# Optimization experiments

Measured on AMD Instinct MI355X. Metric: run time of the kernel, lower is better.

Reference implementation:

```python
import jax, jax.numpy as jnp
import numpy as np

H = 1024
V = 50257
B = 64
T = 512


def setup_inputs() -> dict:
    key = jax.random.key(0)
    ks = jax.random.split(key, 16)
    s = 0.02
    return {
        "input_seq": jax.random.randint(ks[0], (B,), 0, V, dtype=jnp.int32),
        "last_hidden": jax.random.normal(ks[1], (1, B, H), dtype=jnp.float32),
        "encoder_outputs": jax.random.normal(ks[2], (B, T, H), dtype=jnp.float32),
        "emb": jax.random.normal(ks[3], (V, H), dtype=jnp.float32) * s,
        "W_ih": jax.random.normal(ks[4], (3 * H, H), dtype=jnp.float32) * s,
        "W_hh": jax.random.normal(ks[5], (3 * H, H), dtype=jnp.float32) * s,
        "b_ih": jnp.zeros((3 * H,), jnp.float32),
        "b_hh": jnp.zeros((3 * H,), jnp.float32),
        "W_a": jax.random.normal(ks[6], (H, H), dtype=jnp.float32) * s,
        "b_a": jnp.zeros((H,), jnp.float32),
        "W_c": jax.random.normal(ks[7], (H, 2 * H), dtype=jnp.float32) * s,
        "b_c": jnp.zeros((H,), jnp.float32),
        "W_o": jax.random.normal(ks[8], (V, H), dtype=jnp.float32) * s,
        "b_o": jnp.zeros((V,), jnp.float32),
    }


def reference(input_seq, last_hidden, encoder_outputs, emb, W_ih, W_hh, b_ih, b_hh,
              W_a, b_a, W_c, b_c, W_o, b_o):
    # Embedding lookup (dropout is identity in eval)
    x = emb[input_seq]                      # [B, H]
    h0 = last_hidden[0]                     # [B, H] (num_layers == 1)

    # Single GRU step, torch gate order (r, z, n)
    gi = x @ W_ih.T + b_ih                  # [B, 3H]
    gh = h0 @ W_hh.T + b_hh                 # [B, 3H]
    r = jax.nn.sigmoid(gi[:, :H] + gh[:, :H])
    z = jax.nn.sigmoid(gi[:, H:2 * H] + gh[:, H:2 * H])
    n = jnp.tanh(gi[:, 2 * H:] + r * gh[:, 2 * H:])
    h = (1.0 - z) * n + z * h0              # [B, H]

    # Attention, method='general': batched (replaces per-batch torch.mm loop)
    energy = jnp.einsum('bth,oh->bto', encoder_outputs, W_a) + b_a  # [B, T, H]
    scores = jnp.einsum('bh,bth->bt', h, energy)                    # [B, T]
    attn_w = jax.nn.softmax(scores, axis=1)                         # [B, T]
    context = jnp.einsum('bt,bth->bh', attn_w, encoder_outputs)     # [B, H]

    concat_input = jnp.concatenate([h, context], axis=1)            # [B, 2H]
    concat_output = jnp.tanh(concat_input @ W_c.T + b_c)            # [B, H]
    output = concat_output @ W_o.T + b_o                            # [B, V]
    hidden = h[None]                                                # [1, B, H]
    return (output, hidden)
```

## Files before the change

### kernel.cpp

```cpp
#include <hip/hip_runtime.h>
#include <hip/hip_bf16.h>
#include <cstdint>
#include <cstddef>

#define H 1024
#define V 50257
#define B 64
#define T 512

typedef __attribute__((ext_vector_type(8))) short bf16x8;
typedef __attribute__((ext_vector_type(4))) float f32x4;

__device__ __forceinline__ float sigmoidf_(float x) { return 1.0f / (1.0f + expf(-x)); }

__device__ __forceinline__ unsigned short f2bf_rn(float x) {
    __hip_bfloat16 h = __float2bfloat16(x);
    return __builtin_bit_cast(unsigned short, h);
}

__device__ __forceinline__ void gl_lds16(const float* g, float* l) {
    __builtin_amdgcn_global_load_lds(
        (const __attribute__((address_space(1))) unsigned*)g,
        (__attribute__((address_space(3))) unsigned*)l, 16, 0, 0);
}

__device__ __forceinline__ void wait_vm8() {
    asm volatile("s_waitcnt vmcnt(8)" ::: "memory");
    __builtin_amdgcn_sched_barrier(0);
}
__device__ __forceinline__ void wait_vm0() {
    asm volatile("s_waitcnt vmcnt(0)" ::: "memory");
    __builtin_amdgcn_sched_barrier(0);
}
__device__ __forceinline__ void lds_war_guard() {
    asm volatile("s_waitcnt lgkmcnt(0)" ::: "memory");
    __builtin_amdgcn_sched_barrier(0);
}

__global__ __launch_bounds__(256) void k_gates(const int* __restrict__ seq,
                                               const float* __restrict__ emb,
                                               const float* __restrict__ h0,
                                               const float* __restrict__ Wih,
                                               const float* __restrict__ Whh,
                                               float* __restrict__ Pgi,
                                               float* __restrict__ Pgh) {
    __shared__ __align__(16) float Bs[2][128 * 64];
    const int z = blockIdx.z;
    const float* Bm = z ? Whh : Wih;
    float* C = (z ? Pgh : Pgi) + (size_t)blockIdx.y * 64 * (3 * H);
    const int t = threadIdx.x;
    const int w = t >> 6, lane = t & 63;
    const int li = lane & 15, qu = lane >> 4;
    const int n0 = blockIdx.x * 128;
    const int k0 = blockIdx.y * 256;
    const int N = 3 * H;

    const float* Arow[4];
#pragma unroll
    for (int ms = 0; ms < 4; ++ms) {
        int m = ms * 16 + li;
        Arow[ms] = z ? (h0 + (size_t)m * H) : (emb + (size_t)seq[m] * H);
    }

    f32x4 acc[4][2];
#pragma unroll
    for (int ms = 0; ms < 4; ++ms)
#pragma unroll
        for (int nt = 0; nt < 2; ++nt) acc[ms][nt] = (f32x4){0.f, 0.f, 0.f, 0.f};

#define STG(BUF, KK)                                                            \
    {                                                                           \
        _Pragma("unroll")                                                       \
        for (int j = 0; j < 8; ++j) {                                           \
            int cidx = (w * 8 + j) * 64 + lane;                                 \
            int row = cidx >> 4, cs = cidx & 15;                                \
            int cg = cs ^ (row & 15);                                           \
            const float* gp = Bm + (size_t)(n0 + row) * H + (KK) + cg * 4;      \
            gl_lds16(gp, &Bs[BUF][(w * 8 + j) * 256]);                          \
        }                                                                       \
    }

#define CONSUME(BUF, KK)                                                        \
    {                                                                           \
        _Pragma("unroll")                                                       \
        for (int ks = 0; ks < 2; ++ks) {                                        \
            bf16x8 af[4];                                                       \
            _Pragma("unroll")                                                   \
            for (int ms = 0; ms < 4; ++ms) {                                    \
                float4 a0 = *(const float4*)&Arow[ms][(KK) + ks * 32 + qu * 8]; \
                float4 a1 = *(const float4*)&Arow[ms][(KK) + ks * 32 + qu * 8 + 4]; \
                af[ms][0] = (short)f2bf_rn(a0.x); af[ms][1] = (short)f2bf_rn(a0.y); \
                af[ms][2] = (short)f2bf_rn(a0.z); af[ms][3] = (short)f2bf_rn(a0.w); \
                af[ms][4] = (short)f2bf_rn(a1.x); af[ms][5] = (short)f2bf_rn(a1.y); \
                af[ms][6] = (short)f2bf_rn(a1.z); af[ms][7] = (short)f2bf_rn(a1.w); \
            }                                                                   \
            _Pragma("unroll")                                                   \
            for (int nt = 0; nt < 2; ++nt) {                                    \
                int row = w * 32 + nt * 16 + li;                                \
                int cc0 = ks * 8 + qu * 2;                                      \
                float4 x0 = *(const float4*)&Bs[BUF][row * 64 + ((cc0)     ^ (row & 15)) * 4]; \
                float4 x1 = *(const float4*)&Bs[BUF][row * 64 + ((cc0 + 1) ^ (row & 15)) * 4]; \
                bf16x8 bfr;                                                     \
                bfr[0] = (short)f2bf_rn(x0.x); bfr[1] = (short)f2bf_rn(x0.y);   \
                bfr[2] = (short)f2bf_rn(x0.z); bfr[3] = (short)f2bf_rn(x0.w);   \
                bfr[4] = (short)f2bf_rn(x1.x); bfr[5] = (short)f2bf_rn(x1.y);   \
                bfr[6] = (short)f2bf_rn(x1.z); bfr[7] = (short)f2bf_rn(x1.w);   \
                _Pragma("unroll")                                               \
                for (int ms = 0; ms < 4; ++ms)                                  \
                    acc[ms][nt] = __builtin_amdgcn_mfma_f32_16x16x32_bf16(      \
                        af[ms], bfr, acc[ms][nt], 0, 0, 0);                     \
            }                                                                   \
        }                                                                       \
    }

    STG(0, k0)
    STG(1, k0 + 64)
    for (int kt = 0; kt < 3; ++kt) {
        const int buf = kt & 1;
        wait_vm8();
        CONSUME(buf, k0 + kt * 64)
        if (kt + 2 < 4) { lds_war_guard(); STG(buf, k0 + (kt + 2) * 64) }
    }
    wait_vm0();
    CONSUME(1, k0 + 3 * 64)
#undef STG
#undef CONSUME

#pragma unroll
    for (int nt = 0; nt < 2; ++nt) {
        int col = n0 + w * 32 + nt * 16 + li;
#pragma unroll
        for (int ms = 0; ms < 4; ++ms)
#pragma unroll
            for (int j = 0; j < 4; ++j)
                C[(size_t)(ms * 16 + qu * 4 + j) * N + col] = acc[ms][nt][j];
    }
}

__global__ __launch_bounds__(256) void k_mfma_bt(const unsigned short* __restrict__ A,
                                                 int lda,
                                                 const float* __restrict__ Bm, int ldb,
                                                 float* __restrict__ Cp, int N, int KC) {
    __shared__ __align__(16) float Bs[2][128 * 64];
    float* C = Cp + (size_t)blockIdx.y * 64 * N;
    const int t = threadIdx.x;
    const int w = t >> 6, lane = t & 63;
    const int li = lane & 15, qu = lane >> 4;
    const int n0 = blockIdx.x * 128;
    const int k0 = blockIdx.y * KC;
    const int nsteps = KC >> 6;

    f32x4 acc[4][2];
#pragma unroll
    for (int ms = 0; ms < 4; ++ms)
#pragma unroll
        for (int nt = 0; nt < 2; ++nt) acc[ms][nt] = (f32x4){0.f, 0.f, 0.f, 0.f};

#define STG(BUF, KK)                                                            \
    {                                                                           \
        _Pragma("unroll")                                                       \
        for (int j = 0; j < 8; ++j) {                                           \
            int cidx = (w * 8 + j) * 64 + lane;                                 \
            int row = cidx >> 4, cs = cidx & 15;                                \
            int cg = cs ^ (row & 15);                                           \
            const float* gp = Bm + (size_t)(n0 + row) * ldb + (KK) + cg * 4;    \
            gl_lds16(gp, &Bs[BUF][(w * 8 + j) * 256]);                          \
        }                                                                       \
    }

#define CONSUME(BUF, KK)                                                        \
    {                                                                           \
        _Pragma("unroll")                                                       \
        for (int ks = 0; ks < 2; ++ks) {                                        \
            bf16x8 af[4];                                                       \
            _Pragma("unroll")                                                   \
            for (int ms = 0; ms < 4; ++ms)                                      \
                af[ms] = *(const bf16x8*)&A[(size_t)(ms * 16 + li) * lda + (KK) + ks * 32 + qu * 8]; \
            _Pragma("unroll")                                                   \
            for (int nt = 0; nt < 2; ++nt) {                                    \
                int row = w * 32 + nt * 16 + li;                                \
                int cc0 = ks * 8 + qu * 2;                                      \
                float4 x0 = *(const float4*)&Bs[BUF][row * 64 + ((cc0)     ^ (row & 15)) * 4]; \
                float4 x1 = *(const float4*)&Bs[BUF][row * 64 + ((cc0 + 1) ^ (row & 15)) * 4]; \
                bf16x8 bfr;                                                     \
                bfr[0] = (short)f2bf_rn(x0.x); bfr[1] = (short)f2bf_rn(x0.y);   \
                bfr[2] = (short)f2bf_rn(x0.z); bfr[3] = (short)f2bf_rn(x0.w);   \
                bfr[4] = (short)f2bf_rn(x1.x); bfr[5] = (short)f2bf_rn(x1.y);   \
                bfr[6] = (short)f2bf_rn(x1.z); bfr[7] = (short)f2bf_rn(x1.w);   \
                _Pragma("unroll")                                               \
                for (int ms = 0; ms < 4; ++ms)                                  \
                    acc[ms][nt] = __builtin_amdgcn_mfma_f32_16x16x32_bf16(      \
                        af[ms], bfr, acc[ms][nt], 0, 0, 0);                     \
            }                                                                   \
        }                                                                       \
    }

    STG(0, k0)
    STG(1, k0 + 64)
    for (int kt = 0; kt < nsteps - 1; ++kt) {
        const int buf = kt & 1;
        wait_vm8();
        CONSUME(buf, k0 + kt * 64)
        if (kt + 2 < nsteps) { lds_war_guard(); STG(buf, k0 + (kt + 2) * 64) }
    }
    wait_vm0();
    CONSUME((nsteps - 1) & 1, k0 + (nsteps - 1) * 64)
#undef STG
#undef CONSUME

#pragma unroll
    for (int nt = 0; nt < 2; ++nt) {
        int col = n0 + w * 32 + nt * 16 + li;
#pragma unroll
        for (int ms = 0; ms < 4; ++ms)
#pragma unroll
            for (int j = 0; j < 4; ++j)
                C[(size_t)(ms * 16 + qu * 4 + j) * N + col] = acc[ms][nt][j];
    }
}

__global__ __launch_bounds__(256) void k_mfma_wa(const unsigned short* __restrict__ cat_bf,
                                                 const float* __restrict__ Wa,
                                                 float* __restrict__ Pu) {
    const int t = threadIdx.x;
    const int w = t >> 6, lane = t & 63;
    const int li = lane & 15, qu = lane >> 4;
    const int n0 = blockIdx.x * 64;
    const int k0 = blockIdx.y * 128;

    f32x4 acc[4];
#pragma unroll
    for (int ms = 0; ms < 4; ++ms) acc[ms] = (f32x4){0.f, 0.f, 0.f, 0.f};

    const int col = n0 + w * 16 + li;

    for (int kt = 0; kt < 2; ++kt) {
        const int kk = k0 + kt * 64;
#pragma unroll
        for (int ks = 0; ks < 2; ++ks) {
            bf16x8 af[4];
#pragma unroll
            for (int ms = 0; ms < 4; ++ms)
                af[ms] = *(const bf16x8*)&cat_bf[(size_t)(ms * 16 + li) * 2048 + kk + ks * 32 + qu * 8];
            const int kb = kk + ks * 32 + qu * 8;
            bf16x8 bfr;
#pragma unroll
            for (int e = 0; e < 8; ++e)
                bfr[e] = (short)f2bf_rn(Wa[(size_t)(kb + e) * H + col]);
#pragma unroll
            for (int ms = 0; ms < 4; ++ms)
                acc[ms] = __builtin_amdgcn_mfma_f32_16x16x32_bf16(
                    af[ms], bfr, acc[ms], 0, 0, 0);
        }
    }
    float* C = Pu + (size_t)blockIdx.y * 64 * H;
#pragma unroll
    for (int ms = 0; ms < 4; ++ms)
#pragma unroll
        for (int j = 0; j < 4; ++j)
            C[(size_t)(ms * 16 + qu * 4 + j) * H + col] = acc[ms][j];
}

__global__ void k_gru(const float* __restrict__ Pgi, const float* __restrict__ Pgh,
                      const float* __restrict__ bih, const float* __restrict__ bhh,
                      const float* __restrict__ h0, unsigned short* __restrict__ cat_bf,
                      float* __restrict__ hid) {
    int i = blockIdx.x * 256 + threadIdx.x;
    int b = i >> 10, h = i & 1023;
    float gr = bih[h], gz = bih[H + h], gn = bih[2 * H + h];
    float hr = bhh[h], hz = bhh[H + h], hn = bhh[2 * H + h];
#pragma unroll
    for (int kt = 0; kt < 4; ++kt) {
        const float* pi = Pgi + (size_t)kt * B * 3 * H + (size_t)b * 3 * H;
        const float* ph = Pgh + (size_t)kt * B * 3 * H + (size_t)b * 3 * H;
        gr += pi[h]; gz += pi[H + h]; gn += pi[2 * H + h];
        hr += ph[h]; hz += ph[H + h]; hn += ph[2 * H + h];
    }
    float r = sigmoidf_(gr + hr);
    float z = sigmoidf_(gz + hz);
    float n = tanhf(gn + r * hn);
    float hv = (1.0f - z) * n + z * h0[i];
    cat_bf[(size_t)b * 2048 + h] = f2bf_rn(hv);
    hid[i] = hv;
}

__global__ __launch_bounds__(256) void k_flash(const float* __restrict__ Pu,
                                               const float* __restrict__ enc,
                                               float* __restrict__ Pm,
                                               float* __restrict__ Pl,
                                               float* __restrict__ Pc) {
    const int b = blockIdx.x >> 4, ch = blockIdx.x & 15;
    const int w = threadIdx.x >> 6, lane = threadIdx.x & 63;

    float4 uu[4];
#pragma unroll
    for (int it = 0; it < 4; ++it) {
        int col = (it * 64 + lane) * 4;
        float4 s = *(const float4*)&Pu[(size_t)b * H + col];
#pragma unroll
        for (int kt = 1; kt < 8; ++kt) {
            float4 p = *(const float4*)&Pu[(size_t)kt * B * H + (size_t)b * H + col];
            s.x += p.x; s.y += p.y; s.z += p.z; s.w += p.w;
        }
        uu[it] = s;
    }

    float m = -3.4e38f, l = 0.f;
    float4 c[4] = {{0,0,0,0},{0,0,0,0},{0,0,0,0},{0,0,0,0}};
    const float* ebase = enc + ((size_t)b * T + ch * 32 + w * 8) * H;

#pragma unroll 2
    for (int tt = 0; tt < 8; ++tt) {
        float4 e[4];
#pragma unroll
        for (int it = 0; it < 4; ++it)
            e[it] = *(const float4*)&ebase[(size_t)tt * H + (it * 64 + lane) * 4];
        float s = 0.f;
#pragma unroll
        for (int it = 0; it < 4; ++it)
            s += uu[it].x * e[it].x + uu[it].y * e[it].y +
                 uu[it].z * e[it].z + uu[it].w * e[it].w;
#pragma unroll
        for (int o = 32; o; o >>= 1) s += __shfl_xor(s, o, 64);
        float mn = fmaxf(m, s);
        float scale = __expf(m - mn);
        float p = __expf(s - mn);
        l = l * scale + p;
#pragma unroll
        for (int it = 0; it < 4; ++it) {
            c[it].x = fmaf(p, e[it].x, c[it].x * scale);
            c[it].y = fmaf(p, e[it].y, c[it].y * scale);
            c[it].z = fmaf(p, e[it].z, c[it].z * scale);
            c[it].w = fmaf(p, e[it].w, c[it].w * scale);
        }
        m = mn;
    }

    __shared__ float Lm[4], Ll[4];
    __shared__ __align__(16) float Lc[4][H];
#pragma unroll
    for (int it = 0; it < 4; ++it)
        *(float4*)&Lc[w][(it * 64 + lane) * 4] = c[it];
    if (lane == 0) { Lm[w] = m; Ll[w] = l; }
    __syncthreads();

    float M = fmaxf(fmaxf(Lm[0], Lm[1]), fmaxf(Lm[2], Lm[3]));
    float e0 = __expf(Lm[0] - M), e1 = __expf(Lm[1] - M),
          e2 = __expf(Lm[2] - M), e3 = __expf(Lm[3] - M);
    float L = Ll[0] * e0 + Ll[1] * e1 + Ll[2] * e2 + Ll[3] * e3;
    int col = threadIdx.x * 4;
    float4 c0 = *(const float4*)&Lc[0][col];
    float4 c1 = *(const float4*)&Lc[1][col];
    float4 c2 = *(const float4*)&Lc[2][col];
    float4 c3 = *(const float4*)&Lc[3][col];
    float4 cc;
    cc.x = c0.x * e0 + c1.x * e1 + c2.x * e2 + c3.x * e3;
    cc.y = c0.y * e0 + c1.y * e1 + c2.y * e2 + c3.y * e3;
    cc.z = c0.z * e0 + c1.z * e1 + c2.z * e2 + c3.z * e3;
    cc.w = c0.w * e0 + c1.w * e1 + c2.w * e2 + c3.w * e3;
    const int rec = blockIdx.x;
    if (threadIdx.x == 0) { Pm[rec] = M; Pl[rec] = L; }
    *(float4*)&Pc[(size_t)rec * H + col] = cc;
}

__global__ void k_fcomb(const float* __restrict__ Pm, const float* __restrict__ Pl,
                        const float* __restrict__ Pc, unsigned short* __restrict__ cat_bf) {
    const int b = blockIdx.x;
    const int col = threadIdx.x * 4;
    float M = -3.4e38f;
#pragma unroll
    for (int i = 0; i < 16; ++i) M = fmaxf(M, Pm[b * 16 + i]);
    float L = 0.f;
    float4 cc = {0, 0, 0, 0};
#pragma unroll 4
    for (int i = 0; i < 16; ++i) {
        float wgt = __expf(Pm[b * 16 + i] - M);
        L += Pl[b * 16 + i] * wgt;
        float4 p = *(const float4*)&Pc[(size_t)(b * 16 + i) * H + col];
        cc.x += wgt * p.x; cc.y += wgt * p.y;
        cc.z += wgt * p.z; cc.w += wgt * p.w;
    }
    float inv = 1.0f / L;
    ushort4 o;
    o.x = f2bf_rn(cc.x * inv); o.y = f2bf_rn(cc.y * inv);
    o.z = f2bf_rn(cc.z * inv); o.w = f2bf_rn(cc.w * inv);
    *(ushort4*)&cat_bf[(size_t)b * 2048 + 1024 + col] = o;
}

__global__ void k_co(const float* __restrict__ Pc, const float* __restrict__ bc,
                     unsigned short* __restrict__ co_bf) {
    int i = blockIdx.x * 256 + threadIdx.x;
    int h = i & 1023;
    float s = bc[h];
#pragma unroll
    for (int kt = 0; kt < 16; ++kt) s += Pc[kt * (B * H) + i];
    co_bf[i] = f2bf_rn(tanhf(s));
}

__global__ __launch_bounds__(256) void k_out_mfma(const unsigned short* __restrict__ co_bf,
                                                  const float* __restrict__ Wo,
                                                  const float* __restrict__ bo,
                                                  float* __restrict__ out) {
    __shared__ __align__(16) float Bs[2][128 * 64];
    const int t = threadIdx.x;
    const int w = t >> 6, lane = t & 63;
    const int li = lane & 15, qu = lane >> 4;
    const int v0 = blockIdx.x * 128;

    f32x4 acc[4][2];
#pragma unroll
    for (int ms = 0; ms < 4; ++ms)
#pragma unroll
        for (int nt = 0; nt < 2; ++nt) acc[ms][nt] = (f32x4){0.f, 0.f, 0.f, 0.f};

#define STAGE(BUF, KK)                                                          \
    {                                                                           \
        _Pragma("unroll")                                                       \
        for (int j = 0; j < 8; ++j) {                                           \
            int cidx = (w * 8 + j) * 64 + lane;                                 \
            int row = cidx >> 4, cs = cidx & 15;                                \
            int cg = cs ^ (row & 15);                                           \
            int vr = v0 + row; if (vr >= V) vr = V - 1;                         \
            const float* gp = Wo + (size_t)vr * H + (KK) + cg * 4;              \
            gl_lds16(gp, &Bs[BUF][(w * 8 + j) * 256]);                          \
        }                                                                       \
    }

#define CONSUME(BUF, KK)                                                        \
    {                                                                           \
        _Pragma("unroll")                                                       \
        for (int ks = 0; ks < 2; ++ks) {                                        \
            bf16x8 af[4];                                                       \
            _Pragma("unroll")                                                   \
            for (int ms = 0; ms < 4; ++ms)                                      \
                af[ms] = *(const bf16x8*)&co_bf[(size_t)(ms * 16 + li) * H + (KK) + ks * 32 + qu * 8]; \
            _Pragma("unroll")                                                   \
            for (int nt = 0; nt < 2; ++nt) {                                    \
                int row = w * 32 + nt * 16 + li;                                \
                int cc0 = ks * 8 + qu * 2;                                      \
                float4 x0 = *(const float4*)&Bs[BUF][row * 64 + ((cc0)     ^ (row & 15)) * 4]; \
                float4 x1 = *(const float4*)&Bs[BUF][row * 64 + ((cc0 + 1) ^ (row & 15)) * 4]; \
                bf16x8 bfr;                                                     \
                bfr[0] = (short)f2bf_rn(x0.x); bfr[1] = (short)f2bf_rn(x0.y);   \
                bfr[2] = (short)f2bf_rn(x0.z); bfr[3] = (short)f2bf_rn(x0.w);   \
                bfr[4] = (short)f2bf_rn(x1.x); bfr[5] = (short)f2bf_rn(x1.y);   \
                bfr[6] = (short)f2bf_rn(x1.z); bfr[7] = (short)f2bf_rn(x1.w);   \
                _Pragma("unroll")                                               \
                for (int ms = 0; ms < 4; ++ms)                                  \
                    acc[ms][nt] = __builtin_amdgcn_mfma_f32_16x16x32_bf16(      \
                        af[ms], bfr, acc[ms][nt], 0, 0, 0);                     \
            }                                                                   \
        }                                                                       \
    }

    STAGE(0, 0)
    STAGE(1, 64)
    for (int kt = 0; kt < 15; ++kt) {
        const int buf = kt & 1;
        wait_vm8();
        CONSUME(buf, kt * 64)
        if (kt + 2 < 16) { lds_war_guard(); STAGE(buf, (kt + 2) * 64) }
    }
    wait_vm0();
    CONSUME(1, 15 * 64)
#undef STAGE
#undef CONSUME

#pragma unroll
    for (int nt = 0; nt < 2; ++nt) {
        int v = v0 + w * 32 + nt * 16 + li;
        if (v < V) {
            float bov = bo[v];
#pragma unroll
            for (int ms = 0; ms < 4; ++ms)
#pragma unroll
                for (int j = 0; j < 4; ++j)
                    out[(size_t)(ms * 16 + qu * 4 + j) * V + v] = acc[ms][nt][j] + bov;
        }
    }
}

extern "C" void kernel_launch(void* const* d_in, const int* in_sizes, int n_in,
                              void* d_out, int out_size, void* d_ws, size_t ws_size,
                              hipStream_t stream) {
    (void)in_sizes; (void)n_in; (void)out_size; (void)ws_size;
    const int*   seq = (const int*)d_in[0];
    const float* h0  = (const float*)d_in[1];
    const float* enc = (const float*)d_in[2];
    const float* emb = (const float*)d_in[3];
    const float* Wih = (const float*)d_in[4];
    const float* Whh = (const float*)d_in[5];
    const float* bih = (const float*)d_in[6];
    const float* bhh = (const float*)d_in[7];
    const float* Wa  = (const float*)d_in[8];
    const float* Wc  = (const float*)d_in[10];
    const float* bc  = (const float*)d_in[11];
    const float* Wo  = (const float*)d_in[12];
    const float* bo  = (const float*)d_in[13];

    float* out = (float*)d_out;
    float* hid = out + (size_t)B * V;

    float* ws   = (float*)d_ws;
    float* Pgi  = ws;
    float* Pgh  = Pgi + 786432;
    float* Pu   = Pgh + 786432;
    float* Pm   = Pu + 524288;
    float* Pl   = Pm + 1024;
    float* Pc   = Pl + 1024;
    float* Pcg  = Pc + 1048576;
    unsigned short* cat_bf = (unsigned short*)(Pcg + 1048576);
    unsigned short* co_bf  = cat_bf + 131072;

    k_gates<<<dim3(24, 4, 2), 256, 0, stream>>>(seq, emb, h0, Wih, Whh, Pgi, Pgh);
    k_gru<<<256, 256, 0, stream>>>(Pgi, Pgh, bih, bhh, h0, cat_bf, hid);
    k_mfma_wa<<<dim3(16, 8), 256, 0, stream>>>(cat_bf, Wa, Pu);
    k_flash<<<1024, 256, 0, stream>>>(Pu, enc, Pm, Pl, Pc);
    k_fcomb<<<64, 256, 0, stream>>>(Pm, Pl, Pc, cat_bf);
    k_mfma_bt<<<dim3(8, 16), 256, 0, stream>>>(cat_bf, 2 * H, Wc, 2 * H, Pcg, H, 128);
    k_co<<<256, 256, 0, stream>>>(Pcg, bc, co_bf);
    k_out_mfma<<<(V + 127) / 128, 256, 0, stream>>>(co_bf, Wo, bo, out);
}
```

Before: 135.2 us.

## Fuse split-K reductions into producer kernels via last-block atomic counters

The flash-attention partial combine is merged into the flash kernel, and the Wc split-K reduction plus tanh into the Wc GEMM. In each case the last block to finish, detected with an atomic counter after a threadfence, does the combine. This removes two kernel launches and their launch gaps. The cost is a memset for the flags and a serialized tail in the last-arriving block.

```diff
diff --git a/kernel.cpp b/kernel.cpp
--- a/kernel.cpp
+++ b/kernel.cpp
@@ -137,18 +137,192 @@
     }
 }
 
-__global__ __launch_bounds__(256) void k_mfma_bt(const unsigned short* __restrict__ A,
-                                                 int lda,
-                                                 const float* __restrict__ Bm, int ldb,
-                                                 float* __restrict__ Cp, int N, int KC) {
+__global__ void k_gru(const float* __restrict__ Pgi, const float* __restrict__ Pgh,
+                      const float* __restrict__ bih, const float* __restrict__ bhh,
+                      const float* __restrict__ h0, unsigned short* __restrict__ cat_bf,
+                      float* __restrict__ hid) {
+    int i = blockIdx.x * 256 + threadIdx.x;
+    int b = i >> 10, h = i & 1023;
+    float gr = bih[h], gz = bih[H + h], gn = bih[2 * H + h];
+    float hr = bhh[h], hz = bhh[H + h], hn = bhh[2 * H + h];
+#pragma unroll
+    for (int kt = 0; kt < 4; ++kt) {
+        const float* pi = Pgi + (size_t)kt * B * 3 * H + (size_t)b * 3 * H;
+        const float* ph = Pgh + (size_t)kt * B * 3 * H + (size_t)b * 3 * H;
+        gr += pi[h]; gz += pi[H + h]; gn += pi[2 * H + h];
+        hr += ph[h]; hz += ph[H + h]; hn += ph[2 * H + h];
+    }
+    float r = sigmoidf_(gr + hr);
+    float z = sigmoidf_(gz + hz);
+    float n = tanhf(gn + r * hn);
+    float hv = (1.0f - z) * n + z * h0[i];
+    cat_bf[(size_t)b * 2048 + h] = f2bf_rn(hv);
+    hid[i] = hv;
+}
+
+__global__ __launch_bounds__(256) void k_mfma_wa(const unsigned short* __restrict__ cat_bf,
+                                                 const float* __restrict__ Wa,
+                                                 float* __restrict__ Pu) {
+    const int t = threadIdx.x;
+    const int w = t >> 6, lane = t & 63;
+    const int li = lane & 15, qu = lane >> 4;
+    const int n0 = blockIdx.x * 64;
+    const int k0 = blockIdx.y * 128;
+
+    f32x4 acc[4];
+#pragma unroll
+    for (int ms = 0; ms < 4; ++ms) acc[ms] = (f32x4){0.f, 0.f, 0.f, 0.f};
+
+    const int col = n0 + w * 16 + li;
+
+    for (int kt = 0; kt < 2; ++kt) {
+        const int kk = k0 + kt * 64;
+#pragma unroll
+        for (int ks = 0; ks < 2; ++ks) {
+            bf16x8 af[4];
+#pragma unroll
+            for (int ms = 0; ms < 4; ++ms)
+                af[ms] = *(const bf16x8*)&cat_bf[(size_t)(ms * 16 + li) * 2048 + kk + ks * 32 + qu * 8];
+            const int kb = kk + ks * 32 + qu * 8;
+            bf16x8 bfr;
+#pragma unroll
+            for (int e = 0; e < 8; ++e)
+                bfr[e] = (short)f2bf_rn(Wa[(size_t)(kb + e) * H + col]);
+#pragma unroll
+            for (int ms = 0; ms < 4; ++ms)
+                acc[ms] = __builtin_amdgcn_mfma_f32_16x16x32_bf16(
+                    af[ms], bfr, acc[ms], 0, 0, 0);
+        }
+    }
+    float* C = Pu + (size_t)blockIdx.y * 64 * H;
+#pragma unroll
+    for (int ms = 0; ms < 4; ++ms)
+#pragma unroll
+        for (int j = 0; j < 4; ++j)
+            C[(size_t)(ms * 16 + qu * 4 + j) * H + col] = acc[ms][j];
+}
+
+__global__ __launch_bounds__(256) void k_flash_fc(const float* __restrict__ Pu,
+                                                  const float* __restrict__ enc,
+                                                  float* __restrict__ Pm,
+                                                  float* __restrict__ Pl,
+                                                  float* __restrict__ Pc,
+                                                  unsigned short* __restrict__ cat_bf,
+                                                  int* __restrict__ flags) {
+    const int b = blockIdx.x >> 4, ch = blockIdx.x & 15;
+    const int w = threadIdx.x >> 6, lane = threadIdx.x & 63;
+
+    float4 uu[4];
+#pragma unroll
+    for (int it = 0; it < 4; ++it) {
+        int col = (it * 64 + lane) * 4;
+        float4 s = *(const float4*)&Pu[(size_t)b * H + col];
+#pragma unroll
+        for (int kt = 1; kt < 8; ++kt) {
+            float4 p = *(const float4*)&Pu[(size_t)kt * B * H + (size_t)b * H + col];
+            s.x += p.x; s.y += p.y; s.z += p.z; s.w += p.w;
+        }
+        uu[it] = s;
+    }
+
+    float m = -3.4e38f, l = 0.f;
+    float4 c[4] = {{0,0,0,0},{0,0,0,0},{0,0,0,0},{0,0,0,0}};
+    const float* ebase = enc + ((size_t)b * T + ch * 32 + w * 8) * H;
+
+#pragma unroll 2
+    for (int tt = 0; tt < 8; ++tt) {
+        float4 e[4];
+#pragma unroll
+        for (int it = 0; it < 4; ++it)
+            e[it] = *(const float4*)&ebase[(size_t)tt * H + (it * 64 + lane) * 4];
+        float s = 0.f;
+#pragma unroll
+        for (int it = 0; it < 4; ++it)
+            s += uu[it].x * e[it].x + uu[it].y * e[it].y +
+                 uu[it].z * e[it].z + uu[it].w * e[it].w;
+#pragma unroll
+        for (int o = 32; o; o >>= 1) s += __shfl_xor(s, o, 64);
+        float mn = fmaxf(m, s);
+        float scale = __expf(m - mn);
+        float p = __expf(s - mn);
+        l = l * scale + p;
+#pragma unroll
+        for (int it = 0; it < 4; ++it) {
+            c[it].x = fmaf(p, e[it].x, c[it].x * scale);
+            c[it].y = fmaf(p, e[it].y, c[it].y * scale);
+            c[it].z = fmaf(p, e[it].z, c[it].z * scale);
+            c[it].w = fmaf(p, e[it].w, c[it].w * scale);
+        }
+        m = mn;
+    }
+
+    __shared__ float Lm[4], Ll[4];
+    __shared__ __align__(16) float Lc[4][H];
+    __shared__ int isLast;
+#pragma unroll
+    for (int it = 0; it < 4; ++it)
+        *(float4*)&Lc[w][(it * 64 + lane) * 4] = c[it];
+    if (lane == 0) { Lm[w] = m; Ll[w] = l; }
+    __syncthreads();
+
+    float M = fmaxf(fmaxf(Lm[0], Lm[1]), fmaxf(Lm[2], Lm[3]));
+    float e0 = __expf(Lm[0] - M), e1 = __expf(Lm[1] - M),
+          e2 = __expf(Lm[2] - M), e3 = __expf(Lm[3] - M);
+    float L = Ll[0] * e0 + Ll[1] * e1 + Ll[2] * e2 + Ll[3] * e3;
+    int col = threadIdx.x * 4;
+    float4 c0 = *(const float4*)&Lc[0][col];
+    float4 c1 = *(const float4*)&Lc[1][col];
+    float4 c2 = *(const float4*)&Lc[2][col];
+    float4 c3 = *(const float4*)&Lc[3][col];
+    float4 cc;
+    cc.x = c0.x * e0 + c1.x * e1 + c2.x * e2 + c3.x * e3;
+    cc.y = c0.y * e0 + c1.y * e1 + c2.y * e2 + c3.y * e3;
+    cc.z = c0.z * e0 + c1.z * e1 + c2.z * e2 + c3.z * e3;
+    cc.w = c0.w * e0 + c1.w * e1 + c2.w * e2 + c3.w * e3;
+    const int rec = blockIdx.x;
+    if (threadIdx.x == 0) { Pm[rec] = M; Pl[rec] = L; }
+    *(float4*)&Pc[(size_t)rec * H + col] = cc;
+
+    __threadfence();
+    if (threadIdx.x == 0)
+        isLast = (atomicAdd(&flags[b], 1) == 15);
+    __syncthreads();
+    if (!isLast) return;
+    __threadfence();
+
+    float Mg = -3.4e38f;
+#pragma unroll
+    for (int i = 0; i < 16; ++i) Mg = fmaxf(Mg, Pm[b * 16 + i]);
+    float Lg = 0.f;
+    float4 ccg = {0, 0, 0, 0};
+#pragma unroll 4
+    for (int i = 0; i < 16; ++i) {
+        float wgt = __expf(Pm[b * 16 + i] - Mg);
+        Lg += Pl[b * 16 + i] * wgt;
+        float4 p = *(const float4*)&Pc[(size_t)(b * 16 + i) * H + col];
+        ccg.x += wgt * p.x; ccg.y += wgt * p.y;
+        ccg.z += wgt * p.z; ccg.w += wgt * p.w;
+    }
+    float inv = 1.0f / Lg;
+    ushort4 o;
+    o.x = f2bf_rn(ccg.x * inv); o.y = f2bf_rn(ccg.y * inv);
+    o.z = f2bf_rn(ccg.z * inv); o.w = f2bf_rn(ccg.w * inv);
+    *(ushort4*)&cat_bf[(size_t)b * 2048 + 1024 + col] = o;
+}
+
+__global__ __launch_bounds__(256) void k_wc_co(const unsigned short* __restrict__ A,
+                                               const float* __restrict__ Wc,
+                                               const float* __restrict__ bc,
+                                               float* __restrict__ Pcg,
+                                               unsigned short* __restrict__ co_bf,
+                                               int* __restrict__ flags) {
     __shared__ __align__(16) float Bs[2][128 * 64];
-    float* C = Cp + (size_t)blockIdx.y * 64 * N;
+    float* C = Pcg + (size_t)blockIdx.y * 64 * H;
     const int t = threadIdx.x;
     const int w = t >> 6, lane = t & 63;
     const int li = lane & 15, qu = lane >> 4;
     const int n0 = blockIdx.x * 128;
-    const int k0 = blockIdx.y * KC;
-    const int nsteps = KC >> 6;
+    const int k0 = blockIdx.y * 128;
 
     f32x4 acc[4][2];
 #pragma unroll
@@ -163,7 +337,7 @@
             int cidx = (w * 8 + j) * 64 + lane;                                 \
             int row = cidx >> 4, cs = cidx & 15;                                \
             int cg = cs ^ (row & 15);                                           \
-            const float* gp = Bm + (size_t)(n0 + row) * ldb + (KK) + cg * 4;    \
+            const float* gp = Wc + (size_t)(n0 + row) * (2 * H) + (KK) + cg * 4; \
             gl_lds16(gp, &Bs[BUF][(w * 8 + j) * 256]);                          \
         }                                                                       \
     }
@@ -175,7 +349,7 @@
             bf16x8 af[4];                                                       \
             _Pragma("unroll")                                                   \
             for (int ms = 0; ms < 4; ++ms)                                      \
-                af[ms] = *(const bf16x8*)&A[(size_t)(ms * 16 + li) * lda + (KK) + ks * 32 + qu * 8]; \
+                af[ms] = *(const bf16x8*)&A[(size_t)(ms * 16 + li) * 2048 + (KK) + ks * 32 + qu * 8]; \
             _Pragma("unroll")                                                   \
             for (int nt = 0; nt < 2; ++nt) {                                    \
                 int row = w * 32 + nt * 16 + li;                                \
@@ -197,14 +371,10 @@
 
     STG(0, k0)
     STG(1, k0 + 64)
-    for (int kt = 0; kt < nsteps - 1; ++kt) {
-        const int buf = kt & 1;
-        wait_vm8();
-        CONSUME(buf, k0 + kt * 64)
-        if (kt + 2 < nsteps) { lds_war_guard(); STG(buf, k0 + (kt + 2) * 64) }
-    }
+    wait_vm8();
+    CONSUME(0, k0)
     wait_vm0();
-    CONSUME((nsteps - 1) & 1, k0 + (nsteps - 1) * 64)
+    CONSUME(1, k0 + 64)
 #undef STG
 #undef CONSUME
 
@@ -215,186 +385,28 @@
         for (int ms = 0; ms < 4; ++ms)
 #pragma unroll
             for (int j = 0; j < 4; ++j)
-                C[(size_t)(ms * 16 + qu * 4 + j) * N + col] = acc[ms][nt][j];
-    }
-}
-
-__global__ __launch_bounds__(256) void k_mfma_wa(const unsigned short* __restrict__ cat_bf,
-                                                 const float* __restrict__ Wa,
-                                                 float* __restrict__ Pu) {
-    const int t = threadIdx.x;
-    const int w = t >> 6, lane = t & 63;
-    const int li = lane & 15, qu = lane >> 4;
-    const int n0 = blockIdx.x * 64;
-    const int k0 = blockIdx.y * 128;
-
-    f32x4 acc[4];
-#pragma unroll
-    for (int ms = 0; ms < 4; ++ms) acc[ms] = (f32x4){0.f, 0.f, 0.f, 0.f};
-
-    const int col = n0 + w * 16 + li;
-
-    for (int kt = 0; kt < 2; ++kt) {
-        const int kk = k0 + kt * 64;
-#pragma unroll
-        for (int ks = 0; ks < 2; ++ks) {
-            bf16x8 af[4];
-#pragma unroll
-            for (int ms = 0; ms < 4; ++ms)
-                af[ms] = *(const bf16x8*)&cat_bf[(size_t)(ms * 16 + li) * 2048 + kk + ks * 32 + qu * 8];
-            const int kb = kk + ks * 32 + qu * 8;
-            bf16x8 bfr;
-#pragma unroll
-            for (int e = 0; e < 8; ++e)
-                bfr[e] = (short)f2bf_rn(Wa[(size_t)(kb + e) * H + col]);
-#pragma unroll
-            for (int ms = 0; ms < 4; ++ms)
-                acc[ms] = __builtin_amdgcn_mfma_f32_16x16x32_bf16(
-                    af[ms], bfr, acc[ms], 0, 0, 0);
-        }
-    }
-    float* C = Pu + (size_t)blockIdx.y * 64 * H;
-#pragma unroll
-    for (int ms = 0; ms < 4; ++ms)
-#pragma unroll
-        for (int j = 0; j < 4; ++j)
-            C[(size_t)(ms * 16 + qu * 4 + j) * H + col] = acc[ms][j];
-}
-
-__global__ void k_gru(const float* __restrict__ Pgi, const float* __restrict__ Pgh,
-                      const float* __restrict__ bih, const float* __restrict__ bhh,
-                      const float* __restrict__ h0, unsigned short* __restrict__ cat_bf,
-                      float* __restrict__ hid) {
-    int i = blockIdx.x * 256 + threadIdx.x;
-    int b = i >> 10, h = i & 1023;
-    float gr = bih[h], gz = bih[H + h], gn = bih[2 * H + h];
-    float hr = bhh[h], hz = bhh[H + h], hn = bhh[2 * H + h];
-#pragma unroll
-    for (int kt = 0; kt < 4; ++kt) {
-        const float* pi = Pgi + (size_t)kt * B * 3 * H + (size_t)b * 3 * H;
-        const float* ph = Pgh + (size_t)kt * B * 3 * H + (size_t)b * 3 * H;
-        gr += pi[h]; gz += pi[H + h]; gn += pi[2 * H + h];
-        hr += ph[h]; hz += ph[H + h]; hn += ph[2 * H + h];
-    }
-    float r = sigmoidf_(gr + hr);
-    float z = sigmoidf_(gz + hz);
-    float n = tanhf(gn + r * hn);
-    float hv = (1.0f - z) * n + z * h0[i];
-    cat_bf[(size_t)b * 2048 + h] = f2bf_rn(hv);
-    hid[i] = hv;
-}
-
-__global__ __launch_bounds__(256) void k_flash(const float* __restrict__ Pu,
-                                               const float* __restrict__ enc,
-                                               float* __restrict__ Pm,
-                                               float* __restrict__ Pl,
-                                               float* __restrict__ Pc) {
-    const int b = blockIdx.x >> 4, ch = blockIdx.x & 15;
-    const int w = threadIdx.x >> 6, lane = threadIdx.x & 63;
-
-    float4 uu[4];
-#pragma unroll
-    for (int it = 0; it < 4; ++it) {
-        int col = (it * 64 + lane) * 4;
-        float4 s = *(const float4*)&Pu[(size_t)b * H + col];
-#pragma unroll
-        for (int kt = 1; kt < 8; ++kt) {
-            float4 p = *(const float4*)&Pu[(size_t)kt * B * H + (size_t)b * H + col];
-            s.x += p.x; s.y += p.y; s.z += p.z; s.w += p.w;
-        }
-        uu[it] = s;
-    }
-
-    float m = -3.4e38f, l = 0.f;
-    float4 c[4] = {{0,0,0,0},{0,0,0,0},{0,0,0,0},{0,0,0,0}};
-    const float* ebase = enc + ((size_t)b * T + ch * 32 + w * 8) * H;
-
-#pragma unroll 2
-    for (int tt = 0; tt < 8; ++tt) {
-        float4 e[4];
-#pragma unroll
-        for (int it = 0; it < 4; ++it)
-            e[it] = *(const float4*)&ebase[(size_t)tt * H + (it * 64 + lane) * 4];
-        float s = 0.f;
-#pragma unroll
-        for (int it = 0; it < 4; ++it)
-            s += uu[it].x * e[it].x + uu[it].y * e[it].y +
-                 uu[it].z * e[it].z + uu[it].w * e[it].w;
-#pragma unroll
-        for (int o = 32; o; o >>= 1) s += __shfl_xor(s, o, 64);
-        float mn = fmaxf(m, s);
-        float scale = __expf(m - mn);
-        float p = __expf(s - mn);
-        l = l * scale + p;
-#pragma unroll
-        for (int it = 0; it < 4; ++it) {
-            c[it].x = fmaf(p, e[it].x, c[it].x * scale);
-            c[it].y = fmaf(p, e[it].y, c[it].y * scale);
-            c[it].z = fmaf(p, e[it].z, c[it].z * scale);
-            c[it].w = fmaf(p, e[it].w, c[it].w * scale);
-        }
-        m = mn;
-    }
-
-    __shared__ float Lm[4], Ll[4];
-    __shared__ __align__(16) float Lc[4][H];
-#pragma unroll
-    for (int it = 0; it < 4; ++it)
-        *(float4*)&Lc[w][(it * 64 + lane) * 4] = c[it];
-    if (lane == 0) { Lm[w] = m; Ll[w] = l; }
+                C[(size_t)(ms * 16 + qu * 4 + j) * H + col] = acc[ms][nt][j];
+    }
+
+    __shared__ int isLast;
+    __threadfence();
+    if (t == 0)
+        isLast = (atomicAdd(&flags[blockIdx.x], 1) == 15);
     __syncthreads();
-
-    float M = fmaxf(fmaxf(Lm[0], Lm[1]), fmaxf(Lm[2], Lm[3]));
-    float e0 = __expf(Lm[0] - M), e1 = __expf(Lm[1] - M),
-          e2 = __expf(Lm[2] - M), e3 = __expf(Lm[3] - M);
-    float L = Ll[0] * e0 + Ll[1] * e1 + Ll[2] * e2 + Ll[3] * e3;
-    int col = threadIdx.x * 4;
-    float4 c0 = *(const float4*)&Lc[0][col];
-    float4 c1 = *(const float4*)&Lc[1][col];
-    float4 c2 = *(const float4*)&Lc[2][col];
-    float4 c3 = *(const float4*)&Lc[3][col];
-    float4 cc;
-    cc.x = c0.x * e0 + c1.x * e1 + c2.x * e2 + c3.x * e3;
-    cc.y = c0.y * e0 + c1.y * e1 + c2.y * e2 + c3.y * e3;
-    cc.z = c0.z * e0 + c1.z * e1 + c2.z * e2 + c3.z * e3;
-    cc.w = c0.w * e0 + c1.w * e1 + c2.w * e2 + c3.w * e3;
-    const int rec = blockIdx.x;
-    if (threadIdx.x == 0) { Pm[rec] = M; Pl[rec] = L; }
-    *(float4*)&Pc[(size_t)rec * H + col] = cc;
-}
-
-__global__ void k_fcomb(const float* __restrict__ Pm, const float* __restrict__ Pl,
-                        const float* __restrict__ Pc, unsigned short* __restrict__ cat_bf) {
-    const int b = blockIdx.x;
-    const int col = threadIdx.x * 4;
-    float M = -3.4e38f;
-#pragma unroll
-    for (int i = 0; i < 16; ++i) M = fmaxf(M, Pm[b * 16 + i]);
-    float L = 0.f;
-    float4 cc = {0, 0, 0, 0};
+    if (!isLast) return;
+    __threadfence();
+
+#pragma unroll
+    for (int e = 0; e < 32; ++e) {
+        int elem = e * 256 + t;
+        int m_ = elem >> 7, c_ = elem & 127;
+        int n = n0 + c_;
+        float s = bc[n];
 #pragma unroll 4
-    for (int i = 0; i < 16; ++i) {
-        float wgt = __expf(Pm[b * 16 + i] - M);
-        L += Pl[b * 16 + i] * wgt;
-        float4 p = *(const float4*)&Pc[(size_t)(b * 16 + i) * H + col];
-        cc.x += wgt * p.x; cc.y += wgt * p.y;
-        cc.z += wgt * p.z; cc.w += wgt * p.w;
-    }
-    float inv = 1.0f / L;
-    ushort4 o;
-    o.x = f2bf_rn(cc.x * inv); o.y = f2bf_rn(cc.y * inv);
-    o.z = f2bf_rn(cc.z * inv); o.w = f2bf_rn(cc.w * inv);
-    *(ushort4*)&cat_bf[(size_t)b * 2048 + 1024 + col] = o;
-}
-
-__global__ void k_co(const float* __restrict__ Pc, const float* __restrict__ bc,
-                     unsigned short* __restrict__ co_bf) {
-    int i = blockIdx.x * 256 + threadIdx.x;
-    int h = i & 1023;
-    float s = bc[h];
-#pragma unroll
-    for (int kt = 0; kt < 16; ++kt) s += Pc[kt * (B * H) + i];
-    co_bf[i] = f2bf_rn(tanhf(s));
+        for (int kt = 0; kt < 16; ++kt)
+            s += Pcg[(size_t)kt * B * H + (size_t)m_ * H + n];
+        co_bf[(size_t)m_ * H + n] = f2bf_rn(tanhf(s));
+    }
 }
 
 __global__ __launch_bounds__(256) void k_out_mfma(const unsigned short* __restrict__ co_bf,
@@ -511,13 +523,14 @@
     float* Pcg  = Pc + 1048576;
     unsigned short* cat_bf = (unsigned short*)(Pcg + 1048576);
     unsigned short* co_bf  = cat_bf + 131072;
+    int* flags  = (int*)(co_bf + 65536);
+
+    hipMemsetAsync(flags, 0, 72 * sizeof(int), stream);
 
     k_gates<<<dim3(24, 4, 2), 256, 0, stream>>>(seq, emb, h0, Wih, Whh, Pgi, Pgh);
     k_gru<<<256, 256, 0, stream>>>(Pgi, Pgh, bih, bhh, h0, cat_bf, hid);
     k_mfma_wa<<<dim3(16, 8), 256, 0, stream>>>(cat_bf, Wa, Pu);
-    k_flash<<<1024, 256, 0, stream>>>(Pu, enc, Pm, Pl, Pc);
-    k_fcomb<<<64, 256, 0, stream>>>(Pm, Pl, Pc, cat_bf);
-    k_mfma_bt<<<dim3(8, 16), 256, 0, stream>>>(cat_bf, 2 * H, Wc, 2 * H, Pcg, H, 128);
-    k_co<<<256, 256, 0, stream>>>(Pcg, bc, co_bf);
+    k_flash_fc<<<1024, 256, 0, stream>>>(Pu, enc, Pm, Pl, Pc, cat_bf, flags);
+    k_wc_co<<<dim3(8, 16), 256, 0, stream>>>(cat_bf, Wc, bc, Pcg, co_bf, flags + 64);
     k_out_mfma<<<(V + 127) / 128, 256, 0, stream>>>(co_bf, Wo, bo, out);
 }
```

Result: slower. 447.8 us (+231.3%).
